# Kernel optimization log

Measured on AMD Instinct MI355X. Metric: run time of the kernel, lower is better.

The kernel has to match this reference:

```python
import jax, jax.numpy as jnp
import numpy as np

NH = 8          # n_heads
EPS = 1e-12     # layer_norm_eps


def _ln(x, g, b, eps=EPS):
    m = x.mean(-1, keepdims=True)
    v = jnp.var(x, axis=-1, keepdims=True)
    return (x - m) / jnp.sqrt(v + eps) * g + b


def _heads(x):
    # [B,S,H] -> [B,NH,S,H/NH]
    B, S, H = x.shape
    return x.reshape(B, S, NH, H // NH).transpose(0, 2, 1, 3)


def setup_inputs() -> dict:
    B, S, H, INNER = 32, 512, 512, 2048
    n_items = 50000
    std = 0.02
    ks = list(jax.random.split(jax.random.key(0), 20))
    inp = {}
    inp['x'] = jax.random.normal(ks[0], (B, S, H), jnp.float32)
    inp['value_input'] = jax.random.normal(ks[1], (B, S, H), jnp.float32)
    inp['beha_emb'] = jax.random.normal(ks[2], (B, S, H), jnp.float32)
    inp['pos_table'] = std * jax.random.normal(ks[3], (S, H), jnp.float32)
    names = ['q', 'k', 'v', 'pk', 'pq', 'bk', 'bq', 'd']
    for i, n in enumerate(names):
        inp['W' + n] = std * jax.random.normal(ks[4 + i], (H, H), jnp.float32)
        inp['b' + n] = jnp.zeros((H,), jnp.float32)
    inp['ln_g'] = jnp.ones((H,), jnp.float32)
    inp['ln_b'] = jnp.zeros((H,), jnp.float32)
    inp['W1'] = std * jax.random.normal(ks[12], (H, INNER), jnp.float32)
    inp['b1'] = jnp.zeros((INNER,), jnp.float32)
    inp['W2'] = std * jax.random.normal(ks[13], (INNER, H), jnp.float32)
    inp['b2'] = jnp.zeros((H,), jnp.float32)
    inp['ln2_g'] = jnp.ones((H,), jnp.float32)
    inp['ln2_b'] = jnp.zeros((H,), jnp.float32)
    inp['item_seq'] = jax.random.randint(ks[14], (B, S), 0, n_items, jnp.int32)
    return inp


def reference(x, value_input, beha_emb, pos_table, Wq, bq, Wk, bk, Wv, bv,
              Wpk, bpk, Wpq, bpq, Wbk, bbk, Wbq, bbq, Wd, bd, ln_g, ln_b,
              W1, b1, W2, b2, ln2_g, ln2_b, item_seq):
    B, S, H = x.shape
    dh = H // NH
    pos = pos_table[:S][None]  # [1,S,H] position_embedding(arange(S))

    q = _heads(x @ Wq + bq)
    k = _heads(x @ Wk + bk)
    v = _heads(value_input @ Wv + bv + value_input)  # value(value_input) + value_input
    pk = _heads(jnp.broadcast_to(pos @ Wpk + bpk, (B, S, H)))
    pq = _heads(jnp.broadcast_to(pos @ Wpq + bpq, (B, S, H)))
    bhk = _heads(beha_emb @ Wbk + bbk)
    bhq = _heads(beha_emb @ Wbq + bbq)

    # disentangled score: q.k^T + q.((beha_k+pos_k)/2)^T + ((beha_q+pos_q)/2).k^T
    scores = (jnp.einsum('bhqd,bhkd->bhqk', q, k)
              + jnp.einsum('bhqd,bhkd->bhqk', q, (bhk + pk) * 0.5)
              + jnp.einsum('bhqd,bhkd->bhqk', (bhq + pq) * 0.5, k))
    scores = scores / (dh ** 0.5)

    # causal + padding mask: (1 - mask) * -10000
    valid = item_seq > 0                              # [B,S]
    causal = jnp.tril(jnp.ones((S, S), bool))         # [S,S]
    ok = valid[:, None, None, :] & causal[None, None]
    scores = scores + jnp.where(ok, 0.0, -10000.0)

    probs = jax.nn.softmax(scores, axis=-1)
    ctx = jnp.einsum('bhqk,bhkd->bhqd', probs, v)
    ctx = ctx.transpose(0, 2, 1, 3).reshape(B, S, H)

    attn_out = _ln(ctx @ Wd + bd + x, ln_g, ln_b)

    # FeedForward (RecBole): dense1 -> gelu -> dense2 -> LN(residual)
    h = jax.nn.gelu(attn_out @ W1 + b1, approximate=False)
    h = h @ W2 + b2
    return _ln(h + attn_out, ln2_g, ln2_b)
```

## Files before the change

### kernel.cpp

```cpp
#include <hip/hip_runtime.h>
#include <math.h>


typedef unsigned short u16;
typedef __attribute__((ext_vector_type(8))) short bf16x8;
typedef __attribute__((ext_vector_type(4))) float f32x4;

#define NM 16384

__device__ __forceinline__ u16 f2b(float f) {
  union { float f; unsigned u; } x; x.f = f;
  return (u16)((x.u + 0x7fffu + ((x.u >> 16) & 1u)) >> 16);
}
__device__ __forceinline__ float b2f(u16 u) {
  union { unsigned u; float f; } x; x.u = ((unsigned)u) << 16; return x.f;
}
__device__ __forceinline__ f32x4 mfma16(bf16x8 a, bf16x8 b, f32x4 c) {
  return __builtin_amdgcn_mfma_f32_16x16x32_bf16(a, b, c, 0, 0, 0);
}
__device__ __forceinline__ void gl16(const u16* g, u16* l) {
  __builtin_amdgcn_global_load_lds(
      (const __attribute__((address_space(1))) unsigned int*)(const void*)g,
      (__attribute__((address_space(3))) unsigned int*)(void*)l, 16, 0, 0);
}
__device__ __forceinline__ bf16x8 baddv(bf16x8 a, bf16x8 b) {
  bf16x8 r;
  #pragma unroll
  for (int e = 0; e < 8; ++e) r[e] = (short)f2b(b2f((u16)a[e]) + b2f((u16)b[e]));
  return r;
}

__device__ __forceinline__ void kloop(
    const u16* __restrict__ A, const u16* __restrict__ W,
    int m0, int n0, int K, int kiters, u16* sm, bool vres,
    f32x4 (&acc)[4][4])
{
  const int tid = threadIdx.x;
  const int wave = tid>>6, lane = tid&63, quad = lane>>4, l16 = lane&15;
  const int wm = wave>>1, wn = wave&1;
  const int r1 = tid>>2;
  const int ch1 = (((tid&3) ^ ((r1>>1)&3)) << 3);
  const int qsw = ((quad ^ ((l16>>1)&3)) << 3);
  const u16* pA = A + (size_t)(m0+r1)*K + ch1;
  const u16* pB = W + (size_t)(n0+r1)*K + ch1;
  u16* s0 = sm + tid*8;
  gl16(pA, s0);            gl16(pA + (size_t)64*K, s0 + 2048);
  gl16(pB, s0 + 4096);     gl16(pB + (size_t)64*K, s0 + 6144);
  if (kiters > 1) {
    u16* s1 = s0 + 8192;
    gl16(pA + 32, s1);          gl16(pA + (size_t)64*K + 32, s1 + 2048);
    gl16(pB + 32, s1 + 4096);   gl16(pB + (size_t)64*K + 32, s1 + 6144);
    asm volatile("s_waitcnt vmcnt(4)" ::: "memory");
  } else {
    asm volatile("s_waitcnt vmcnt(0)" ::: "memory");
  }
  __builtin_amdgcn_s_barrier();
  int buf = 0;
  for (int it = 0; it < kiters; ++it) {
    if (it + 2 < kiters) {
      const int kn = (it + 2)*32;
      int nb = buf - 1; if (nb < 0) nb += 3;
      u16* sn = s0 + nb*8192;
      gl16(pA + kn, sn);           gl16(pA + (size_t)64*K + kn, sn + 2048);
      gl16(pB + kn, sn + 4096);    gl16(pB + (size_t)64*K + kn, sn + 6144);
    }
    const u16* As = sm + buf*8192;
    const u16* Bs = As + 4096;
    bf16x8 af[4], bf[4];
    #pragma unroll
    for (int i = 0; i < 4; ++i)
      af[i] = *(const bf16x8*)&As[(wm*64 + i*16 + l16)*32 + qsw];
    #pragma unroll
    for (int j = 0; j < 4; ++j)
      bf[j] = *(const bf16x8*)&Bs[(wn*64 + j*16 + l16)*32 + qsw];
    if (vres) {
      const int k0 = it*32;
      #pragma unroll
      for (int j = 0; j < 4; ++j) {
        const int start = n0 + wn*64 + j*16;
        if ((start & ~31) == k0) {
          const int c = (start & 31) + l16;
          #pragma unroll
          for (int i = 0; i < 4; ++i)
            #pragma unroll
            for (int rr = 0; rr < 4; ++rr) {
              const int rw = wm*64 + i*16 + quad*4 + rr;
              const int sw = ((((c>>3) ^ ((rw>>1)&3)) << 3) | (c & 7));
              acc[i][j][rr] += b2f(As[rw*32 + sw]);
            }
        }
      }
    }
    __builtin_amdgcn_s_setprio(1);
    #pragma unroll
    for (int i = 0; i < 4; ++i)
      #pragma unroll
      for (int j = 0; j < 4; ++j)
        acc[i][j] = mfma16(af[i], bf[j], acc[i][j]);
    __builtin_amdgcn_s_setprio(0);
    if (it + 2 < kiters)
      asm volatile("s_waitcnt vmcnt(4)" ::: "memory");
    else
      asm volatile("s_waitcnt vmcnt(0)" ::: "memory");
    __builtin_amdgcn_s_barrier();
    buf = (buf + 1 == 3) ? 0 : buf + 1;
  }
}

__device__ __forceinline__ void epi_std(
    f32x4 (&acc)[4][4], const float* __restrict__ bias,
    const u16* __restrict__ ex, int exmode, float scale, int gelu,
    u16* __restrict__ out, int m0, int n0, int N, u16* til)
{
  const int tid = threadIdx.x;
  const int wave = tid>>6, lane = tid&63, quad = lane>>4, l16 = lane&15;
  const int wm = wave>>1, wn = wave&1;
  #pragma unroll
  for (int pass = 0; pass < 2; ++pass) {
    if (wm == pass) {
      #pragma unroll
      for (int j = 0; j < 4; ++j) {
        const int c = wn*64 + j*16 + l16;
        const float bv = bias[n0 + c];
        #pragma unroll
        for (int i = 0; i < 4; ++i)
          #pragma unroll
          for (int rr = 0; rr < 4; ++rr) {
            float v = acc[i][j][rr] + bv;
            if (gelu) v = 0.5f*v*(1.0f + erff(v*0.70710678118654752f));
            til[(i*16 + quad*4 + rr)*136 + c] = f2b(v);
          }
      }
    }
    __syncthreads();
    const int r = tid>>2, ck = tid&3;
    const int gr = m0 + pass*64 + r;
    #pragma unroll
    for (int kk = 0; kk < 4; ++kk) {
      const int cc = ck*32 + kk*8, gc = n0 + cc;
      u16 e8[8];
      *(uint4*)e8 = *(const uint4*)&til[r*136 + cc];
      if (exmode) {
        const u16* ep = (exmode == 1) ? &ex[(size_t)(gr & 511)*512 + gc]
                                      : &ex[(size_t)gr*512 + gc];
        #pragma unroll
        for (int e = 0; e < 8; ++e) e8[e] = f2b((b2f(e8[e]) + b2f(ep[e]))*scale);
      } else if (scale != 1.0f) {
        #pragma unroll
        for (int e = 0; e < 8; ++e) e8[e] = f2b(b2f(e8[e])*scale);
      }
      *(uint4*)&out[(size_t)gr*N + gc] = *(uint4*)e8;
    }
    __syncthreads();
  }
}

__device__ __forceinline__ void epi_vt(
    f32x4 (&acc)[4][4], const float* __restrict__ bias,
    u16* __restrict__ Vt, int m0, int n0, u16* til)
{
  const int tid = threadIdx.x;
  const int wave = tid>>6, lane = tid&63, quad = lane>>4, l16 = lane&15;
  const int wm = wave>>1, wn = wave&1;
  const int b = m0 >> 9, s0 = m0 & 511;
  #pragma unroll
  for (int pass = 0; pass < 2; ++pass) {
    if (wn == pass) {
      #pragma unroll
      for (int j = 0; j < 4; ++j) {
        const int cl = j*16 + l16;
        const float bv = bias[n0 + pass*64 + cl];
        #pragma unroll
        for (int i = 0; i < 4; ++i)
          #pragma unroll
          for (int rr = 0; rr < 4; ++rr)
            til[cl*136 + wm*64 + i*16 + quad*4 + rr] = f2b(acc[i][j][rr] + bv);
      }
    }
    __syncthreads();
    const int cl = tid>>2, ck = tid&3;
    const int gn = n0 + pass*64 + cl, h = gn>>6, d = gn&63;
    u16* orow = Vt + ((size_t)((b*8 + h)*64 + d))*512 + s0 + ck*32;
    #pragma unroll
    for (int kk = 0; kk < 4; ++kk)
      *(uint4*)&orow[kk*8] = *(const uint4*)&til[cl*136 + ck*32 + kk*8];
    __syncthreads();
  }
}

struct PJ { const u16* A; const u16* W; const float* bias; const u16* ex;
            u16* out; float scale; int exmode; int epiv; };
struct ProjArgs { PJ p[7]; };

__global__ __launch_bounds__(256, 2) void proj_kernel(ProjArgs pa, int phaseBase) {
  __shared__ __align__(16) u16 smem[24576];
  const int nbx = gridDim.x;
  const int nwg = nbx * gridDim.y;
  int lin = blockIdx.y*nbx + blockIdx.x;
  lin = (lin & 7)*(nwg >> 3) + (lin >> 3);
  const int bx = lin % nbx, by = lin / nbx;
  const PJ P = pa.p[phaseBase + (bx >> 2)];
  const int n0 = (bx & 3)*128, m0 = by*128;
  f32x4 acc[4][4] = {};
  kloop(P.A, P.W, m0, n0, 512, 16, smem, P.epiv != 0, acc);
  if (P.epiv) epi_vt(acc, P.bias, P.out, m0, n0, smem);
  else        epi_std(acc, P.bias, P.ex, P.exmode, P.scale, 0, P.out, m0, n0, 512, smem);
}

template<int GELU>
__global__ __launch_bounds__(256, 2) void gemm1_kernel(
    const u16* __restrict__ A, const u16* __restrict__ W,
    const float* __restrict__ bias, u16* __restrict__ out, int N, int K)
{
  __shared__ __align__(16) u16 smem[24576];
  const int nbx = gridDim.x;
  const int nwg = nbx * gridDim.y;
  int lin = blockIdx.y*nbx + blockIdx.x;
  lin = (lin & 7)*(nwg >> 3) + (lin >> 3);
  const int m0 = (lin / nbx)*128, n0 = (lin % nbx)*128;
  f32x4 acc[4][4] = {};
  kloop(A, W, m0, n0, K, K>>5, smem, false, acc);
  epi_std(acc, bias, nullptr, 0, 1.0f, GELU, out, m0, n0, N, smem);
}

__global__ __launch_bounds__(256) void cast_all_kernel(
    const float* __restrict__ x, const float* __restrict__ v,
    const float* __restrict__ be, const float* __restrict__ pos,
    u16* __restrict__ xb, u16* __restrict__ vb, u16* __restrict__ bb,
    u16* __restrict__ posb)
{
  int z = blockIdx.y;
  const float* in = (z==0) ? x : (z==1) ? v : (z==2) ? be : pos;
  u16* out = (z==0) ? xb : (z==1) ? vb : (z==2) ? bb : posb;
  int n4 = (z < 3) ? (NM*512/4) : (512*512/4);
  int i = blockIdx.x*256 + threadIdx.x;
  if (i >= n4) return;
  float4 w = ((const float4*)in)[i];
  ((ushort4*)out)[i] = make_ushort4(f2b(w.x), f2b(w.y), f2b(w.z), f2b(w.w));
}

struct PrepArgs {
  const float* w[10];
  u16* o[10];
  const float* bbq; const float* bbk;
  float* Bq2; float* Bk2;
};
__global__ __launch_bounds__(256) void wprep_all_kernel(PrepArgs a) {
  int job = blockIdx.x;
  if (job == 1024) {
    for (int i = threadIdx.x; i < 512; i += 256) {
      a.Bq2[i] = 0.5f*a.bbq[i];
      a.Bk2[i] = 0.5f*a.bbk[i];
    }
    return;
  }
  int wsel, n0, k0, K, N;
  if (job < 512)      { wsel = job>>6; int t = job&63;  n0=(t&7)*64;  k0=(t>>3)*64; K=512;  N=512; }
  else if (job < 768) { wsel = 8;      int t = job-512; n0=(t&31)*64; k0=(t>>5)*64; K=512;  N=2048; }
  else                { wsel = 9;      int t = job-768; n0=(t&7)*64;  k0=(t>>3)*64; K=2048; N=512; }
  float sc = (wsel == 5 || wsel == 6) ? 0.5f : 1.0f;
  const float* in = a.w[wsel];
  u16* out = a.o[wsel];
  __shared__ __align__(16) u16 til[64*72];
  for (int idx = threadIdx.x; idx < 4096; idx += 256) {
    int r = idx>>6, c = idx&63;
    til[r*72+c] = f2b(in[(size_t)(k0+r)*N + n0+c] * sc);
  }
  __syncthreads();
  for (int idx = threadIdx.x; idx < 4096; idx += 256) {
    int r = idx>>6, c = idx&63;
    out[(size_t)(n0+r)*K + k0+c] = til[c*72+r];
  }
}

__global__ __launch_bounds__(512, 2) void attn_kernel(
    const u16* __restrict__ Qraw, const u16* __restrict__ Praw,
    const u16* __restrict__ Kraw, const u16* __restrict__ Mraw,
    const u16* __restrict__ Vt, const int* __restrict__ iseq,
    u16* __restrict__ ctx)
{
  const int qh = blockIdx.x, h = blockIdx.y, b = blockIdx.z;
  const int tid = threadIdx.x;
  const int wave = tid>>6, lane = tid&63, quad = lane>>4, l16 = lane&15;

  __shared__ __align__(16) u16 Ks[2][64*136];
  __shared__ __align__(16) u16 Vs[2][64*72];
  __shared__ __align__(16) u16 Ps[8][16*72];
  __shared__ float sel[512];

  const int q0 = qh*256;
  const int ntiles = 4*qh + 4;
  const u16* Kg = Kraw + (size_t)(b*512)*512 + h*64;
  const u16* Mg = Mraw + (size_t)(b*512)*512 + h*64;
  const u16* Vg = Vt + (size_t)((b*8 + h)*64)*512;

  if (tid < 512) sel[tid] = (iseq[b*512 + tid] > 0) ? 1.0f : 1e-30f;

  bf16x8 aq[2][4];
  #pragma unroll
  for (int s = 0; s < 2; ++s) {
    const size_t ro = (size_t)(b*512 + q0 + s*128 + wave*16 + l16)*512 + h*64;
    bf16x8 qf0 = *(const bf16x8*)&Qraw[ro + quad*8];
    bf16x8 qf1 = *(const bf16x8*)&Qraw[ro + 32 + quad*8];
    bf16x8 pf0 = *(const bf16x8*)&Praw[ro + quad*8];
    bf16x8 pf1 = *(const bf16x8*)&Praw[ro + 32 + quad*8];
    aq[s][0] = baddv(qf0, pf0); aq[s][1] = baddv(qf1, pf1);
    aq[s][2] = qf0;             aq[s][3] = qf1;
  }

  const int sr = tid>>3, sc8 = (tid&7)*8;
  uint4 kreg = *(const uint4*)&Kg[(size_t)sr*512 + sc8];
  uint4 mreg = *(const uint4*)&Mg[(size_t)sr*512 + sc8];
  uint4 vreg = *(const uint4*)&Vg[(size_t)sr*512 + sc8];

  f32x4 Ob[2][4] = {};
  float lrow[2][4] = {};
  u16* Pw = Ps[wave];
  int buf = 0;

  for (int kt = 0; kt < ntiles; ++kt) {
    const int k0 = kt*64;
    *(uint4*)&Ks[buf][sr*136 + sc8]      = kreg;
    *(uint4*)&Ks[buf][sr*136 + 64 + sc8] = mreg;
    *(uint4*)&Vs[buf][sr*72 + sc8]       = vreg;
    __syncthreads();
    if (kt + 1 < ntiles) {
      const int kn = k0 + 64;
      kreg = *(const uint4*)&Kg[(size_t)(kn + sr)*512 + sc8];
      mreg = *(const uint4*)&Mg[(size_t)(kn + sr)*512 + sc8];
      vreg = *(const uint4*)&Vg[(size_t)sr*512 + kn + sc8];
    }
    const bool act0 = (q0 + wave*16 + 15) >= k0;
    const bool act1 = (q0 + 128 + wave*16 + 15) >= k0;
    if (act1) {
      f32x4 sc[2][4] = {};
      #pragma unroll
      for (int ks = 0; ks < 4; ++ks) {
        bf16x8 bk[4];
        #pragma unroll
        for (int j = 0; j < 4; ++j)
          bk[j] = *(const bf16x8*)&Ks[buf][(j*16 + l16)*136 + ks*32 + quad*8];
        if (act0) {
          #pragma unroll
          for (int j = 0; j < 4; ++j) sc[0][j] = mfma16(aq[0][ks], bk[j], sc[0][j]);
        }
        #pragma unroll
        for (int j = 0; j < 4; ++j) sc[1][j] = mfma16(aq[1][ks], bk[j], sc[1][j]);
      }
      #pragma unroll
      for (int s = 0; s < 2; ++s) {
        if (s == 0 && !act0) continue;
        const int rb = q0 + s*128 + wave*16 + quad*4;
        float pj[4][4];
        #pragma unroll
        for (int j = 0; j < 4; ++j) {
          int col = k0 + j*16 + l16;
          float fs = sel[col];
          #pragma unroll
          for (int r = 0; r < 4; ++r) {
            float m2 = (col <= rb + r) ? fs : 1e-30f;
            pj[j][r] = __expf(sc[s][j][r]) * m2;
          }
        }
        #pragma unroll
        for (int r = 0; r < 4; ++r)
          lrow[s][r] += pj[0][r] + pj[1][r] + pj[2][r] + pj[3][r];
        #pragma unroll
        for (int j = 0; j < 4; ++j)
          #pragma unroll
          for (int r = 0; r < 4; ++r)
            Pw[(quad*4 + r)*72 + j*16 + l16] = f2b(pj[j][r]);
        #pragma unroll
        for (int c = 0; c < 4; ++c) {
          #pragma unroll
          for (int k2 = 0; k2 < 2; ++k2) {
            bf16x8 ap = *(const bf16x8*)&Pw[l16*72 + k2*32 + quad*8];
            bf16x8 bv = *(const bf16x8*)&Vs[buf][(c*16 + l16)*72 + k2*32 + quad*8];
            Ob[s][c] = mfma16(ap, bv, Ob[s][c]);
          }
        }
      }
    }
    buf ^= 1;
  }

  #pragma unroll
  for (int s = 0; s < 2; ++s) {
    #pragma unroll
    for (int r = 0; r < 4; ++r) {
      float l = lrow[s][r];
      #pragma unroll
      for (int d2 = 1; d2 < 16; d2 <<= 1) l += __shfl_xor(l, d2, 64);
      float inv = 1.0f / l;
      int grow = b*512 + q0 + s*128 + wave*16 + quad*4 + r;
      #pragma unroll
      for (int c = 0; c < 4; ++c)
        ctx[(size_t)grow*512 + h*64 + c*16 + l16] = f2b(Ob[s][c][r]*inv);
    }
  }
}

template<int RES>
__global__ __launch_bounds__(256) void ln_kernel(
    const u16* __restrict__ a, const void* __restrict__ resv,
    const float* __restrict__ g, const float* __restrict__ be,
    float* __restrict__ of, u16* __restrict__ ob)
{
  const int wave = threadIdx.x >> 6, lane = threadIdx.x & 63;
  const int row = blockIdx.x*4 + wave;
  const ushort4* pa = (const ushort4*)(a + (size_t)row*512);
  ushort4 a0 = pa[lane], a1 = pa[lane+64];
  float v[8] = { b2f(a0.x), b2f(a0.y), b2f(a0.z), b2f(a0.w),
                 b2f(a1.x), b2f(a1.y), b2f(a1.z), b2f(a1.w) };
  if (RES == 1) {
    const ushort4* pr = (const ushort4*)((const u16*)resv + (size_t)row*512);
    ushort4 u0 = pr[lane], u1 = pr[lane+64];
    v[0]+=b2f(u0.x); v[1]+=b2f(u0.y); v[2]+=b2f(u0.z); v[3]+=b2f(u0.w);
    v[4]+=b2f(u1.x); v[5]+=b2f(u1.y); v[6]+=b2f(u1.z); v[7]+=b2f(u1.w);
  } else {
    const float4* pr = (const float4*)((const float*)resv + (size_t)row*512);
    float4 r0 = pr[lane], r1 = pr[lane+64];
    v[0]+=r0.x; v[1]+=r0.y; v[2]+=r0.z; v[3]+=r0.w;
    v[4]+=r1.x; v[5]+=r1.y; v[6]+=r1.z; v[7]+=r1.w;
  }
  float s = 0.f, q = 0.f;
  #pragma unroll
  for (int e = 0; e < 8; ++e) { s += v[e]; q += v[e]*v[e]; }
  #pragma unroll
  for (int d = 1; d < 64; d <<= 1) { s += __shfl_xor(s, d, 64); q += __shfl_xor(q, d, 64); }
  float mean = s * (1.0f/512.0f);
  float var  = q * (1.0f/512.0f) - mean*mean;
  float rstd = rsqrtf(var + 1e-12f);
  float4 g0 = ((const float4*)g)[lane],  g1 = ((const float4*)g)[lane+64];
  float4 b0 = ((const float4*)be)[lane], b1 = ((const float4*)be)[lane+64];
  float o[8];
  o[0]=(v[0]-mean)*rstd*g0.x+b0.x; o[1]=(v[1]-mean)*rstd*g0.y+b0.y;
  o[2]=(v[2]-mean)*rstd*g0.z+b0.z; o[3]=(v[3]-mean)*rstd*g0.w+b0.w;
  o[4]=(v[4]-mean)*rstd*g1.x+b1.x; o[5]=(v[5]-mean)*rstd*g1.y+b1.y;
  o[6]=(v[6]-mean)*rstd*g1.z+b1.z; o[7]=(v[7]-mean)*rstd*g1.w+b1.w;
  if (of) {
    ((float4*)(of + (size_t)row*512))[lane]    = make_float4(o[0],o[1],o[2],o[3]);
    ((float4*)(of + (size_t)row*512))[lane+64] = make_float4(o[4],o[5],o[6],o[7]);
  }
  if (ob) {
    ((ushort4*)(ob + (size_t)row*512))[lane]    = make_ushort4(f2b(o[0]),f2b(o[1]),f2b(o[2]),f2b(o[3]));
    ((ushort4*)(ob + (size_t)row*512))[lane+64] = make_ushort4(f2b(o[4]),f2b(o[5]),f2b(o[6]),f2b(o[7]));
  }
}

extern "C" void kernel_launch(void* const* d_in, const int* in_sizes, int n_in,
                              void* d_out, int out_size, void* d_ws, size_t ws_size,
                              hipStream_t stream) {
  (void)in_sizes; (void)n_in; (void)out_size; (void)ws_size;
  const float* x    = (const float*)d_in[0];
  const float* vin  = (const float*)d_in[1];
  const float* beh  = (const float*)d_in[2];
  const float* pos  = (const float*)d_in[3];
  const float* bq   = (const float*)d_in[5];
  const float* bk   = (const float*)d_in[7];
  const float* bv   = (const float*)d_in[9];
  const float* bpk  = (const float*)d_in[11];
  const float* bpq  = (const float*)d_in[13];
  const float* bbk  = (const float*)d_in[15];
  const float* bbq  = (const float*)d_in[17];
  const float* bd   = (const float*)d_in[19];
  const float* ln_g = (const float*)d_in[20];
  const float* ln_b = (const float*)d_in[21];
  const float* b1   = (const float*)d_in[23];
  const float* b2   = (const float*)d_in[25];
  const float* ln2_g= (const float*)d_in[26];
  const float* ln2_b= (const float*)d_in[27];
  const int*   iseq = (const int*)d_in[28];
  float* out = (float*)d_out;
  char* ws = (char*)d_ws;

  size_t off = 0;
  auto nxt = [&](size_t sz) { size_t r = off; off += (sz + 255) & ~(size_t)255; return r; };
  size_t oWT[8]; for (int i = 0; i < 8; ++i) oWT[i] = nxt(512*512*2);
  size_t oW1T = nxt((size_t)512*2048*2);
  size_t oW2T = nxt((size_t)512*2048*2);
  size_t oBq2 = nxt(512*4);
  size_t oBk2 = nxt(512*4);
  size_t oPb  = nxt(512*512*2);
  size_t oPQ  = nxt(512*512*2);
  size_t oPK  = nxt(512*512*2);
  size_t oXb  = nxt((size_t)NM*512*2);
  size_t oVb  = nxt((size_t)NM*512*2);
  size_t oBb  = nxt((size_t)NM*512*2);
  size_t oQr  = nxt((size_t)NM*512*2);
  size_t oPr  = nxt((size_t)NM*512*2);
  size_t oKr  = nxt((size_t)NM*512*2);
  size_t oMr  = nxt((size_t)NM*512*2);
  size_t oVt  = nxt((size_t)NM*512*2);

  u16* WT[8]; for (int i = 0; i < 8; ++i) WT[i] = (u16*)(ws + oWT[i]);
  u16*   W1T  = (u16*)(ws + oW1T);
  u16*   W2T  = (u16*)(ws + oW2T);
  float* Bq2  = (float*)(ws + oBq2);
  float* Bk2  = (float*)(ws + oBk2);
  u16*   posb = (u16*)(ws + oPb);
  u16*   PQs  = (u16*)(ws + oPQ);
  u16*   PKs  = (u16*)(ws + oPK);
  u16*   xb   = (u16*)(ws + oXb);
  u16*   vb   = (u16*)(ws + oVb);
  u16*   bb   = (u16*)(ws + oBb);
  u16*   Qraw = (u16*)(ws + oQr);
  u16*   Praw = (u16*)(ws + oPr);
  u16*   Kraw = (u16*)(ws + oKr);
  u16*   Mraw = (u16*)(ws + oMr);
  u16*   Vtb  = (u16*)(ws + oVt);
  u16*   Cb   = (u16*)(ws + oVb);
  u16*   db   = (u16*)(ws + oPr);
  u16*   ab   = (u16*)(ws + oXb);
  u16*   h1b  = (u16*)(ws + oQr);
  u16*   f2   = (u16*)(ws + oVt);

  cast_all_kernel<<<dim3(8192, 4), 256, 0, stream>>>(x, vin, beh, pos, xb, vb, bb, posb);
  PrepArgs pr;
  const int wi[10] = {4, 6, 8, 10, 12, 14, 16, 18, 22, 24};
  for (int i = 0; i < 10; ++i) pr.w[i] = (const float*)d_in[wi[i]];
  for (int i = 0; i < 8; ++i)  pr.o[i] = WT[i];
  pr.o[8] = W1T; pr.o[9] = W2T;
  pr.bbq = bbq; pr.bbk = bbk; pr.Bq2 = Bq2; pr.Bk2 = Bk2;
  wprep_all_kernel<<<1025, 256, 0, stream>>>(pr);
  ProjArgs pj;
  pj.p[0] = { xb,   WT[0], bq,   nullptr, Qraw, 0.125f, 0, 0 };
  pj.p[1] = { xb,   WT[1], bk,   nullptr, Kraw, 1.0f,   0, 0 };
  pj.p[2] = { bb,   WT[6], Bq2,  PQs,     Praw, 0.125f, 1, 0 };
  pj.p[3] = { bb,   WT[5], Bk2,  PKs,     Mraw, 1.0f,   1, 0 };
  pj.p[4] = { vb,   WT[2], bv,   nullptr, Vtb,  1.0f,   0, 1 };
  pj.p[5] = { posb, WT[4], bpq,  nullptr, PQs,  0.5f,   0, 0 };
  pj.p[6] = { posb, WT[3], bpk,  nullptr, PKs,  0.5f,   0, 0 };
  proj_kernel<<<dim3(8, 4), 256, 0, stream>>>(pj, 5);
  proj_kernel<<<dim3(20, 128), 256, 0, stream>>>(pj, 0);
  attn_kernel<<<dim3(2, 8, 32), 512, 0, stream>>>(Qraw, Praw, Kraw, Mraw, Vtb, iseq, Cb);
  gemm1_kernel<0><<<dim3(4, 128), 256, 0, stream>>>(Cb, WT[7], bd, db, 512, 512);
  ln_kernel<0><<<4096, 256, 0, stream>>>(db, x, ln_g, ln_b, nullptr, ab);
  gemm1_kernel<1><<<dim3(16, 128), 256, 0, stream>>>(ab, W1T, b1, h1b, 2048, 512);
  gemm1_kernel<0><<<dim3(4, 128), 256, 0, stream>>>(h1b, W2T, b2, f2, 512, 2048);
  ln_kernel<1><<<4096, 256, 0, stream>>>(f2, ab, ln2_g, ln2_b, out, nullptr);
}
```

Before: 507.0 us.

## Use 256x256 GEMM tiles for projections and FFN1, fold V residual into weights

Adds a 512-thread kernel using 256x256 output tiles (8x4 MFMA accumulators per wave) for the four main projections and the GELU FFN1 GEMM. The larger tiles give more reuse per LDS load and halve global traffic per output, at the cost of more registers, 96KB of LDS and fewer workgroups. The value residual (V = xWv + x) is moved from the per-iteration accumulation inside the GEMM loop into the weight prep by adding the identity to Wv, removing a branch from the inner loop. The V projection keeps the 128-tile kernel and is launched separately.

Measured after the change: 772.5 us. 1.52x slower.

```diff
diff --git a/kernel.cpp b/kernel.cpp
--- a/kernel.cpp
+++ b/kernel.cpp
@@ -32,7 +32,7 @@
 
 __device__ __forceinline__ void kloop(
     const u16* __restrict__ A, const u16* __restrict__ W,
-    int m0, int n0, int K, int kiters, u16* sm, bool vres,
+    int m0, int n0, int K, int kiters, u16* sm,
     f32x4 (&acc)[4][4])
 {
   const int tid = threadIdx.x;
@@ -73,24 +73,6 @@
     #pragma unroll
     for (int j = 0; j < 4; ++j)
       bf[j] = *(const bf16x8*)&Bs[(wn*64 + j*16 + l16)*32 + qsw];
-    if (vres) {
-      const int k0 = it*32;
-      #pragma unroll
-      for (int j = 0; j < 4; ++j) {
-        const int start = n0 + wn*64 + j*16;
-        if ((start & ~31) == k0) {
-          const int c = (start & 31) + l16;
-          #pragma unroll
-          for (int i = 0; i < 4; ++i)
-            #pragma unroll
-            for (int rr = 0; rr < 4; ++rr) {
-              const int rw = wm*64 + i*16 + quad*4 + rr;
-              const int sw = ((((c>>3) ^ ((rw>>1)&3)) << 3) | (c & 7));
-              acc[i][j][rr] += b2f(As[rw*32 + sw]);
-            }
-        }
-      }
-    }
     __builtin_amdgcn_s_setprio(1);
     #pragma unroll
     for (int i = 0; i < 4; ++i)
@@ -104,6 +86,113 @@
       asm volatile("s_waitcnt vmcnt(0)" ::: "memory");
     __builtin_amdgcn_s_barrier();
     buf = (buf + 1 == 3) ? 0 : buf + 1;
+  }
+}
+
+__device__ __forceinline__ void kloop256(
+    const u16* __restrict__ A, const u16* __restrict__ W,
+    int m0, int n0, int K, int kiters, u16* sm,
+    f32x4 (&acc)[8][4])
+{
+  const int tid = threadIdx.x;
+  const int wave = tid>>6, lane = tid&63, quad = lane>>4, l16 = lane&15;
+  const int wm = wave>>2, wn = wave&3;
+  const int r1 = tid>>2;
+  const int ch1 = (((tid&3) ^ ((r1>>1)&3)) << 3);
+  const int qsw = ((quad ^ ((l16>>1)&3)) << 3);
+  const u16* pA = A + (size_t)(m0+r1)*K + ch1;
+  const u16* pB = W + (size_t)(n0+r1)*K + ch1;
+  u16* s0 = sm + tid*8;
+  gl16(pA, s0);             gl16(pA + (size_t)128*K, s0 + 4096);
+  gl16(pB, s0 + 8192);      gl16(pB + (size_t)128*K, s0 + 12288);
+  if (kiters > 1) {
+    u16* s1 = s0 + 16384;
+    gl16(pA + 32, s1);           gl16(pA + (size_t)128*K + 32, s1 + 4096);
+    gl16(pB + 32, s1 + 8192);    gl16(pB + (size_t)128*K + 32, s1 + 12288);
+    asm volatile("s_waitcnt vmcnt(4)" ::: "memory");
+  } else {
+    asm volatile("s_waitcnt vmcnt(0)" ::: "memory");
+  }
+  __builtin_amdgcn_s_barrier();
+  int buf = 0;
+  for (int it = 0; it < kiters; ++it) {
+    if (it + 2 < kiters) {
+      const int kn = (it + 2)*32;
+      int nb = buf - 1; if (nb < 0) nb += 3;
+      u16* sn = s0 + nb*16384;
+      gl16(pA + kn, sn);           gl16(pA + (size_t)128*K + kn, sn + 4096);
+      gl16(pB + kn, sn + 8192);    gl16(pB + (size_t)128*K + kn, sn + 12288);
+    }
+    const u16* As = sm + buf*16384;
+    const u16* Bs = As + 8192;
+    bf16x8 af[8], bf[4];
+    #pragma unroll
+    for (int i = 0; i < 8; ++i)
+      af[i] = *(const bf16x8*)&As[(wm*128 + i*16 + l16)*32 + qsw];
+    #pragma unroll
+    for (int j = 0; j < 4; ++j)
+      bf[j] = *(const bf16x8*)&Bs[(wn*64 + j*16 + l16)*32 + qsw];
+    __builtin_amdgcn_s_setprio(1);
+    #pragma unroll
+    for (int i = 0; i < 8; ++i)
+      #pragma unroll
+      for (int j = 0; j < 4; ++j)
+        acc[i][j] = mfma16(af[i], bf[j], acc[i][j]);
+    __builtin_amdgcn_s_setprio(0);
+    if (it + 2 < kiters)
+      asm volatile("s_waitcnt vmcnt(4)" ::: "memory");
+    else
+      asm volatile("s_waitcnt vmcnt(0)" ::: "memory");
+    __builtin_amdgcn_s_barrier();
+    buf = (buf + 1 == 3) ? 0 : buf + 1;
+  }
+}
+
+template<int GELU>
+__device__ __forceinline__ void epi256(
+    f32x4 (&acc)[8][4], const float* __restrict__ bias,
+    const u16* __restrict__ ex, int exmode, float scale,
+    u16* __restrict__ out, int m0, int n0, int N, u16* til)
+{
+  const int tid = threadIdx.x;
+  const int wave = tid>>6, lane = tid&63, quad = lane>>4, l16 = lane&15;
+  const int wm = wave>>2, wn = wave&3;
+  #pragma unroll
+  for (int pass = 0; pass < 2; ++pass) {
+    if (wm == pass) {
+      #pragma unroll
+      for (int j = 0; j < 4; ++j) {
+        const int c = wn*64 + j*16 + l16;
+        const float bv = bias[n0 + c];
+        #pragma unroll
+        for (int i = 0; i < 8; ++i)
+          #pragma unroll
+          for (int rr = 0; rr < 4; ++rr) {
+            float v = acc[i][j][rr] + bv;
+            if (GELU) v = 0.5f*v*(1.0f + erff(v*0.70710678118654752f));
+            til[(i*16 + quad*4 + rr)*264 + c] = f2b(v);
+          }
+      }
+    }
+    __syncthreads();
+    const int r = tid>>2, ck = tid&3;
+    const int gr = m0 + pass*128 + r;
+    #pragma unroll
+    for (int c8 = 0; c8 < 8; ++c8) {
+      const int cc = (ck + 4*c8)*8, gc = n0 + cc;
+      u16 e8[8];
+      *(uint4*)e8 = *(const uint4*)&til[r*264 + cc];
+      if (exmode) {
+        const u16* ep = &ex[(size_t)(gr & 511)*512 + gc];
+        #pragma unroll
+        for (int e = 0; e < 8; ++e) e8[e] = f2b((b2f(e8[e]) + b2f(ep[e]))*scale);
+      } else if (scale != 1.0f) {
+        #pragma unroll
+        for (int e = 0; e < 8; ++e) e8[e] = f2b(b2f(e8[e])*scale);
+      }
+      *(uint4*)&out[(size_t)gr*N + gc] = *(uint4*)e8;
+    }
+    __syncthreads();
   }
 }
 
@@ -202,9 +291,23 @@
   const PJ P = pa.p[phaseBase + (bx >> 2)];
   const int n0 = (bx & 3)*128, m0 = by*128;
   f32x4 acc[4][4] = {};
-  kloop(P.A, P.W, m0, n0, 512, 16, smem, P.epiv != 0, acc);
+  kloop(P.A, P.W, m0, n0, 512, 16, smem, acc);
   if (P.epiv) epi_vt(acc, P.bias, P.out, m0, n0, smem);
   else        epi_std(acc, P.bias, P.ex, P.exmode, P.scale, 0, P.out, m0, n0, 512, smem);
+}
+
+__global__ __launch_bounds__(512, 2) void proj256_kernel(ProjArgs pa) {
+  __shared__ __align__(16) u16 smem[49152];
+  const int nbx = gridDim.x;
+  const int nwg = nbx * gridDim.y;
+  int lin = blockIdx.y*nbx + blockIdx.x;
+  lin = (lin & 7)*(nwg >> 3) + (lin >> 3);
+  const int bx = lin % nbx, by = lin / nbx;
+  const PJ P = pa.p[bx >> 1];
+  const int n0 = (bx & 1)*256, m0 = by*256;
+  f32x4 acc[8][4] = {};
+  kloop256(P.A, P.W, m0, n0, 512, 16, smem, acc);
+  epi256<0>(acc, P.bias, P.ex, P.exmode, P.scale, P.out, m0, n0, 512, smem);
 }
 
 template<int GELU>
@@ -219,8 +322,24 @@
   lin = (lin & 7)*(nwg >> 3) + (lin >> 3);
   const int m0 = (lin / nbx)*128, n0 = (lin % nbx)*128;
   f32x4 acc[4][4] = {};
-  kloop(A, W, m0, n0, K, K>>5, smem, false, acc);
+  kloop(A, W, m0, n0, K, K>>5, smem, acc);
   epi_std(acc, bias, nullptr, 0, 1.0f, GELU, out, m0, n0, N, smem);
+}
+
+template<int GELU>
+__global__ __launch_bounds__(512, 2) void gemm256_kernel(
+    const u16* __restrict__ A, const u16* __restrict__ W,
+    const float* __restrict__ bias, u16* __restrict__ out, int N, int K)
+{
+  __shared__ __align__(16) u16 smem[49152];
+  const int nbx = gridDim.x;
+  const int nwg = nbx * gridDim.y;
+  int lin = blockIdx.y*nbx + blockIdx.x;
+  lin = (lin & 7)*(nwg >> 3) + (lin >> 3);
+  const int m0 = (lin / nbx)*256, n0 = (lin % nbx)*256;
+  f32x4 acc[8][4] = {};
+  kloop256(A, W, m0, n0, K, K>>5, smem, acc);
+  epi256<GELU>(acc, bias, nullptr, 0, 1.0f, out, m0, n0, N, smem);
 }
 
 __global__ __launch_bounds__(256) void cast_all_kernel(
@@ -264,7 +383,9 @@
   __shared__ __align__(16) u16 til[64*72];
   for (int idx = threadIdx.x; idx < 4096; idx += 256) {
     int r = idx>>6, c = idx&63;
-    til[r*72+c] = f2b(in[(size_t)(k0+r)*N + n0+c] * sc);
+    float val = in[(size_t)(k0+r)*N + n0+c] * sc;
+    if (wsel == 2 && (k0+r) == (n0+c)) val += 1.0f;
+    til[r*72+c] = f2b(val);
   }
   __syncthreads();
   for (int idx = threadIdx.x; idx < 4096; idx += 256) {
@@ -532,11 +653,12 @@
   pj.p[5] = { posb, WT[4], bpq,  nullptr, PQs,  0.5f,   0, 0 };
   pj.p[6] = { posb, WT[3], bpk,  nullptr, PKs,  0.5f,   0, 0 };
   proj_kernel<<<dim3(8, 4), 256, 0, stream>>>(pj, 5);
-  proj_kernel<<<dim3(20, 128), 256, 0, stream>>>(pj, 0);
+  proj256_kernel<<<dim3(8, 64), 512, 0, stream>>>(pj);
+  proj_kernel<<<dim3(4, 128), 256, 0, stream>>>(pj, 4);
   attn_kernel<<<dim3(2, 8, 32), 512, 0, stream>>>(Qraw, Praw, Kraw, Mraw, Vtb, iseq, Cb);
   gemm1_kernel<0><<<dim3(4, 128), 256, 0, stream>>>(Cb, WT[7], bd, db, 512, 512);
   ln_kernel<0><<<4096, 256, 0, stream>>>(db, x, ln_g, ln_b, nullptr, ab);
-  gemm1_kernel<1><<<dim3(16, 128), 256, 0, stream>>>(ab, W1T, b1, h1b, 2048, 512);
+  gemm256_kernel<1><<<dim3(8, 64), 512, 0, stream>>>(ab, W1T, b1, h1b, 2048, 512);
   gemm1_kernel<0><<<dim3(4, 128), 256, 0, stream>>>(h1b, W2T, b2, f2, 512, 2048);
   ln_kernel<1><<<4096, 256, 0, stream>>>(f2, ab, ln2_g, ln2_b, out, nullptr);
 }
```
